# Kernel optimization log

Measured on AMD Instinct MI355X. Metric: run time of the kernel, lower is better.

Reference implementation:

```python
import jax, jax.numpy as jnp
import numpy as np

EPS_CLAMP = 1.0 - 1e-06


def _patch_pool_view(x, H, W, p):
    # x: (n, H*W, s) with spatial flattened row-major over (H, W)
    # -> (n, (H//p)*(W//p), p*p, s), matching einops 'n (h ph w pw) s -> n (h w) (ph pw) s'
    n, q, s = x.shape
    h, w = H // p, W // p
    x = x.reshape(n, h, p, w, p, s)
    x = x.transpose(0, 1, 3, 2, 4, 5)  # n h w ph pw s
    return x.reshape(n, h * w, p * p, s)


def setup_inputs() -> dict:
    key = jax.random.key(0)
    k1, k2 = jax.random.split(key)
    N, C, H, W = 8, 256, 48, 48
    return {
        'mask_feats': jax.random.normal(k1, (N, C, H, W), dtype=jnp.float32),
        'query_feats_all': jax.random.normal(k2, (N, C, H, W), dtype=jnp.float32),
        'path_size': 4,
    }


def reference(mask_feats, query_feats_all, path_size):
    N, c_m, hm, wm = mask_feats.shape
    _, c_q, hq, wq = query_feats_all.shape
    # n c h w -> n (h w) c, scaled by 1/sqrt(c)
    mf = mask_feats.reshape(N, c_m, hm * wm).transpose(0, 2, 1) / (c_m ** 0.5)
    qf = query_feats_all.reshape(N, c_q, hq * wq).transpose(0, 2, 1) / (c_q ** 0.5)
    sim_matrix = jnp.einsum('nqc,nsc->nqs', qf, mf) * 10.0  # (N, Q, S)
    instance_masks = jax.nn.softmax(sim_matrix, axis=1)
    query_masks = jnp.swapaxes(jax.nn.softmax(sim_matrix, axis=2), 1, 2)  # (N, S, Q)
    # patch pooling (computed under torch.no_grad in original)
    tmp_instance_masks_d = jax.lax.stop_gradient(
        _patch_pool_view(instance_masks, hq, wq, path_size))
    instance_masks_d = jnp.minimum(tmp_instance_masks_d.sum(axis=2), EPS_CLAMP)
    tmp_query_masks_d = jax.lax.stop_gradient(
        _patch_pool_view(query_masks, hm, wm, path_size))
    query_masks_d = jnp.minimum(tmp_query_masks_d.sum(axis=2), EPS_CLAMP)
    return (instance_masks, query_masks, instance_masks_d, query_masks_d,
            tmp_instance_masks_d, tmp_query_masks_d)
```

## Files before the change

### kernel.cpp

```cpp
#include <hip/hip_runtime.h>
#include <hip/hip_bf16.h>

#define N_B 8
#define CH 256
#define HW 2304
#define SZ_QS (2304LL*2304LL)
#define SCALE 0.0390625f
#define EPSC 0.999999f
#define QS 512.0f
#define IQS 0.001953125f

typedef __attribute__((ext_vector_type(8))) short bf8_t;
typedef __attribute__((ext_vector_type(8))) unsigned short u16x8;
typedef __attribute__((ext_vector_type(4))) float f32x4;

#define O1 0LL
#define O2 42467328LL
#define O3 84934656LL
#define O4 87588864LL
#define O5 90243072LL
#define O6 132710400LL

__device__ __forceinline__ void gl_lds16(const unsigned short* g, unsigned short* l) {
  __builtin_amdgcn_global_load_lds(
      (const __attribute__((address_space(1))) unsigned int*)g,
      (__attribute__((address_space(3))) unsigned int*)l, 16, 0, 0);
}

__global__ __launch_bounds__(256) void k_tr(const float* __restrict__ q_in,
                                            const float* __restrict__ m_in,
                                            __hip_bfloat16* __restrict__ Abf,
                                            __hip_bfloat16* __restrict__ Bbf,
                                            float* __restrict__ zbuf) {
  __shared__ float lds[64][65];
  const int n = blockIdx.z >> 1, which = blockIdx.z & 1;
  const float* src = which ? m_in : q_in;
  __hip_bfloat16* dst = which ? Bbf : Abf;
  const int q0 = blockIdx.x * 64, c0 = blockIdx.y * 64;
  const int t = threadIdx.x;

  if (zbuf && blockIdx.y == 0 && blockIdx.z == 0) {
    const int i = (blockIdx.x * 256 + t) * 4;
    *(float4*)(zbuf + i) = make_float4(0.f, 0.f, 0.f, 0.f);
  }

  const int cl4 = t >> 4, q4 = (t & 15) * 4;
#pragma unroll
  for (int p = 0; p < 4; ++p) {
    const int cl = p * 16 + cl4;
    const float4 v = *(const float4*)(src + ((size_t)n * CH + c0 + cl) * HW + q0 + q4);
    lds[cl][q4 + 0] = v.x;
    lds[cl][q4 + 1] = v.y;
    lds[cl][q4 + 2] = v.z;
    lds[cl][q4 + 3] = v.w;
  }
  __syncthreads();

  const int c8 = (t & 7) * 8;
#pragma unroll
  for (int p = 0; p < 2; ++p) {
    const int ql = p * 32 + (t >> 3);
    u16x8 o;
#pragma unroll
    for (int k = 0; k < 8; ++k) {
      const __hip_bfloat16 h = __float2bfloat16(lds[c8 + k][ql]);
      o[k] = *(const unsigned short*)&h;
    }
    *(u16x8*)((unsigned short*)dst + ((size_t)n * HW + q0 + ql) * CH + c0 + c8) = o;
  }
}

__global__ __launch_bounds__(256) void k_zero(float* __restrict__ p) {
  const int i = (blockIdx.x * 256 + threadIdx.x) * 4;
  *(float4*)(p + i) = make_float4(0.f, 0.f, 0.f, 0.f);
}

__global__ __launch_bounds__(256) void k_inv(const float* __restrict__ s,
                                             float* __restrict__ inv,
                                             const float scale) {
  const int i = blockIdx.x * 256 + threadIdx.x;
  inv[i] = scale / s[i];
}

__global__ __launch_bounds__(512) void k_p1(
    const unsigned short* __restrict__ Abf, const unsigned short* __restrict__ Bbf,
    float* __restrict__ out1, float* __restrict__ rowsum, float* __restrict__ colsum) {
  __shared__ char smem[49152];
  unsigned short* lA = (unsigned short*)smem;
  unsigned short* lB = (unsigned short*)(smem + 24576);

  const int n = blockIdx.z;
  const int S0 = blockIdx.x * 192, Q0 = blockIdx.y * 192;
  const int t = threadIdx.x, l = t & 63, w = t >> 6;
  const int wm = w >> 2, wn = w & 3;
  const int g = l >> 4, c = l & 15;

  f32x4 acc[6][3];
#pragma unroll
  for (int mi = 0; mi < 6; ++mi)
#pragma unroll
    for (int ni = 0; ni < 3; ++ni) {
      f32x4 z = {0.f, 0.f, 0.f, 0.f};
      acc[mi][ni] = z;
    }

  const int r0w = w * 24;
  const int lrow = l >> 3, lc8 = l & 7;
  const int scol = (lc8 ^ lrow) * 8;
  const unsigned short* gA = Abf + ((size_t)n * HW + Q0 + r0w + lrow) * CH + scol;
  const unsigned short* gB = Bbf + ((size_t)n * HW + S0 + r0w + lrow) * CH + scol;
  unsigned short* dA = lA + r0w * 64;
  unsigned short* dB = lB + r0w * 64;

  for (int kc = 0; kc < 4; ++kc) {
    const int k0 = kc * 64;
    gl_lds16(gA + k0, dA);
    gl_lds16(gA + k0 + 8 * CH, dA + 8 * 64);
    gl_lds16(gA + k0 + 16 * CH, dA + 16 * 64);
    gl_lds16(gB + k0, dB);
    gl_lds16(gB + k0 + 8 * CH, dB + 8 * 64);
    gl_lds16(gB + k0 + 16 * CH, dB + 16 * 64);
    __syncthreads();
#pragma unroll
    for (int ks = 0; ks < 2; ++ks) {
      const int kb = ks * 4 + g;
      bf8_t af[6], bf_[3];
#pragma unroll
      for (int mi = 0; mi < 6; ++mi) {
        const int r = wm * 96 + mi * 16 + c;
        af[mi] = *(const bf8_t*)(lA + r * 64 + ((kb ^ (c & 7)) * 8));
      }
#pragma unroll
      for (int ni = 0; ni < 3; ++ni) {
        const int r = wn * 48 + ni * 16 + c;
        bf_[ni] = *(const bf8_t*)(lB + r * 64 + ((kb ^ (c & 7)) * 8));
      }
#pragma unroll
      for (int mi = 0; mi < 6; ++mi)
#pragma unroll
        for (int ni = 0; ni < 3; ++ni)
          acc[mi][ni] = __builtin_amdgcn_mfma_f32_16x16x32_bf16(af[mi], bf_[ni], acc[mi][ni], 0, 0, 0);
    }
    __syncthreads();
  }

#pragma unroll
  for (int mi = 0; mi < 6; ++mi)
#pragma unroll
    for (int ni = 0; ni < 3; ++ni)
#pragma unroll
      for (int r = 0; r < 4; ++r)
        acc[mi][ni][r] = __expf(acc[mi][ni][r] * SCALE);

  u16x8 ud[9];
#pragma unroll
  for (int mi = 0; mi < 6; ++mi)
#pragma unroll
    for (int ni = 0; ni < 3; ++ni)
#pragma unroll
      for (int r = 0; r < 4; ++r) {
        const int L = mi * 12 + ni * 4 + r;
        ud[L >> 3][L & 7] =
            (unsigned short)fminf(acc[mi][ni][r] * QS + 0.5f, 65535.0f);
      }
  {
    const size_t base = ((size_t)n * HW + Q0) * HW + S0;
#pragma unroll
    for (int j = 0; j < 9; ++j) {
      const int chunk = j * 512 + t;
      const int row = chunk / 48, c16 = chunk % 48;
      *(u16x8*)(out1 + base + (size_t)row * HW + c16 * 4) = ud[j];
    }
  }

#pragma unroll
  for (int mi = 0; mi < 6; ++mi)
#pragma unroll
    for (int r = 0; r < 4; ++r) {
      float v = acc[mi][0][r] + acc[mi][1][r] + acc[mi][2][r];
      v += __shfl_xor(v, 1, 64);
      v += __shfl_xor(v, 2, 64);
      v += __shfl_xor(v, 4, 64);
      v += __shfl_xor(v, 8, 64);
      if (c == 0) atomicAdd(&rowsum[n * HW + Q0 + wm * 96 + mi * 16 + g * 4 + r], v);
    }
#pragma unroll
  for (int ni = 0; ni < 3; ++ni) {
    float v = 0.f;
#pragma unroll
    for (int mi = 0; mi < 6; ++mi)
#pragma unroll
      for (int r = 0; r < 4; ++r) v += acc[mi][ni][r];
    v += __shfl_xor(v, 16, 64);
    v += __shfl_xor(v, 32, 64);
    if (g == 0) atomicAdd(&colsum[n * HW + S0 + wn * 48 + ni * 16 + c], v);
  }
}

__global__ __launch_bounds__(512) void k_p2(
    float* __restrict__ out1, float* __restrict__ out2, float* __restrict__ out3,
    float* __restrict__ out4, float* __restrict__ out5, float* __restrict__ out6,
    const float* __restrict__ rowsum, const float* __restrict__ colsum) {
  __shared__ float fb[48 * 196];
  const int n = blockIdx.z;
  const int bx = blockIdx.x, hq = blockIdx.y;
  const int S0 = bx * 192, Q0 = hq * 192;
  const int t = threadIdx.x, l = t & 63, w = t >> 6;
  const int wm = w >> 2, wn = w & 3;
  const int g = l >> 4, c = l & 15;

  u16x8 ud[9];
  {
    const size_t base = ((size_t)n * HW + Q0) * HW + S0;
#pragma unroll
    for (int j = 0; j < 9; ++j) {
      const int chunk = j * 512 + t;
      const int row = chunk / 48, c16 = chunk % 48;
      ud[j] = *(const u16x8*)(out1 + base + (size_t)row * HW + c16 * 4);
    }
  }
  f32x4 acc[6][3];
#pragma unroll
  for (int mi = 0; mi < 6; ++mi)
#pragma unroll
    for (int ni = 0; ni < 3; ++ni)
#pragma unroll
      for (int r = 0; r < 4; ++r) {
        const int L = mi * 12 + ni * 4 + r;
        acc[mi][ni][r] = (float)ud[L >> 3][L & 7];
      }

  float icv[3];
#pragma unroll
  for (int ni = 0; ni < 3; ++ni)
    icv[ni] = IQS / colsum[n * HW + S0 + wn * 48 + ni * 16 + c];
  f32x4 irv6[6];
#pragma unroll
  for (int mi = 0; mi < 6; ++mi) {
    const int qloc = wm * 96 + mi * 16 + g * 4;
    const f32x4 rs = *(const f32x4*)(rowsum + n * HW + Q0 + qloc);
#pragma unroll
    for (int r = 0; r < 4; ++r) irv6[mi][r] = IQS / rs[r];
  }

#pragma unroll
  for (int ch = 0; ch < 4; ++ch) {
    if (wm == (ch >> 1)) {
#pragma unroll
      for (int m3 = 0; m3 < 3; ++m3) {
        const int mi = (ch & 1) * 3 + m3;
        const int rowb = m3 * 16 + g * 4;
#pragma unroll
        for (int ni = 0; ni < 3; ++ni) {
          const int colb = wn * 48 + ni * 16 + c;
#pragma unroll
          for (int r = 0; r < 4; ++r)
            fb[(rowb + r) * 196 + colb] = acc[mi][ni][r] * icv[ni];
        }
      }
    }
    __syncthreads();
#pragma unroll
    for (int j = 0; j < 5; ++j) {
      const int idx = t + j * 512;
      if (idx < 2304) {
        const int row = idx / 48, col4 = idx % 48;
        const float4 v = *(const float4*)(fb + row * 196 + col4 * 4);
        *(float4*)(out1 + ((size_t)n * HW + Q0 + ch * 48 + row) * HW + S0 + col4 * 4) = v;
        const size_t r5 = ((size_t)n * 144 + hq * 12 + (row >> 2)) * 16 + ch * 4 + (row & 3);
        *(float4*)(out5 + r5 * HW + S0 + col4 * 4) = v;
      }
    }
    __syncthreads();
  }

#pragma unroll
  for (int ch = 0; ch < 4; ++ch) {
    if (wn == ch) {
#pragma unroll
      for (int mi = 0; mi < 6; ++mi) {
        const int colf = wm * 96 + mi * 16 + g * 4;
#pragma unroll
        for (int ni = 0; ni < 3; ++ni) {
          const f32x4 pq = acc[mi][ni] * irv6[mi];
          *(f32x4*)(fb + (ni * 16 + c) * 196 + colf) = pq;
        }
      }
    }
    __syncthreads();
#pragma unroll
    for (int j = 0; j < 5; ++j) {
      const int idx = t + j * 512;
      if (idx < 2304) {
        const int row = idx / 48, col4 = idx % 48;
        const float4 v = *(const float4*)(fb + row * 196 + col4 * 4);
        *(float4*)(out2 + ((size_t)n * HW + S0 + ch * 48 + row) * HW + Q0 + col4 * 4) = v;
        const size_t r6 = ((size_t)n * 144 + bx * 12 + (row >> 2)) * 16 + ch * 4 + (row & 3);
        *(float4*)(out6 + r6 * HW + Q0 + col4 * 4) = v;
      }
    }
    __syncthreads();
  }

#pragma unroll
  for (int m3 = 0; m3 < 3; ++m3) {
    const int b = m3 * 4 + g;
#pragma unroll
    for (int ni = 0; ni < 3; ++ni) {
      const int sl = wn * 48 + ni * 16 + c;
      float p = 0.f;
#pragma unroll
      for (int r = 0; r < 4; ++r) p += acc[m3][ni][r] + acc[m3 + 3][ni][r];
      fb[(wm * 12 + b) * 196 + sl] = p * icv[ni];
    }
  }
  __syncthreads();
#pragma unroll
  for (int j = 0; j < 5; ++j) {
    const int idx = t + j * 512;
    if (idx < 2304) {
      const int b = idx / 192, sl = idx % 192;
      const float v = fb[b * 196 + sl] + fb[(12 + b) * 196 + sl];
      out3[((size_t)n * 144 + hq * 12 + b) * HW + S0 + sl] = fminf(v, EPSC);
    }
  }
  __syncthreads();

#pragma unroll
  for (int mi = 0; mi < 6; ++mi) {
    const int qloc = wm * 96 + mi * 16 + g * 4;
#pragma unroll
    for (int ni = 0; ni < 3; ++ni) {
      f32x4 pq = acc[mi][ni] * irv6[mi];
#pragma unroll
      for (int r = 0; r < 4; ++r) {
        pq[r] += __shfl_xor(pq[r], 1, 64);
        pq[r] += __shfl_xor(pq[r], 2, 64);
      }
      if ((c & 3) == 0) {
        const int pc = ni * 4 + (c >> 2);
        *(f32x4*)(fb + (wn * 12 + pc) * 196 + qloc) = pq;
      }
    }
  }
  __syncthreads();
#pragma unroll
  for (int j = 0; j < 5; ++j) {
    const int idx = t + j * 512;
    if (idx < 2304) {
      const int pc = idx / 192, q = idx % 192;
      const float v = fb[pc * 196 + q] + fb[(12 + pc) * 196 + q] +
                      fb[(24 + pc) * 196 + q] + fb[(36 + pc) * 196 + q];
      out4[((size_t)n * 144 + bx * 12 + pc) * HW + Q0 + q] = fminf(v, EPSC);
    }
  }
}

__global__ __launch_bounds__(256) void k_gemm_old(const unsigned short* __restrict__ Abf,
                                                  const unsigned short* __restrict__ Bbf,
                                                  float* __restrict__ out1,
                                                  float* __restrict__ rowsum,
                                                  float* __restrict__ colsum) {
  __shared__ unsigned short lA[128 * 64];
  __shared__ unsigned short lB[128 * 64];
  const int n = blockIdx.z;
  const int s0 = blockIdx.x * 128, q0 = blockIdx.y * 128;
  const int t = threadIdx.x, l = t & 63, w = t >> 6;
  const int wm = w >> 1, wn = w & 1;
  f32x4 acc[4][4];
#pragma unroll
  for (int mi = 0; mi < 4; ++mi)
#pragma unroll
    for (int ni = 0; ni < 4; ++ni) {
      f32x4 z = {0.f, 0.f, 0.f, 0.f};
      acc[mi][ni] = z;
    }
  const size_t baseA = ((size_t)n * HW + q0) * CH;
  const size_t baseB = ((size_t)n * HW + s0) * CH;
  const int jj = t & 7, rr = t >> 3;
  for (int kc = 0; kc < 4; ++kc) {
    const int k0 = kc * 64;
#pragma unroll
    for (int i = 0; i < 4; ++i) {
      const int r = i * 32 + rr;
      bf8_t va = *(const bf8_t*)(Abf + baseA + (size_t)r * CH + k0 + jj * 8);
      bf8_t vb = *(const bf8_t*)(Bbf + baseB + (size_t)r * CH + k0 + jj * 8);
      *(bf8_t*)(lA + r * 64 + ((jj ^ (r & 7)) * 8)) = va;
      *(bf8_t*)(lB + r * 64 + ((jj ^ (r & 7)) * 8)) = vb;
    }
    __syncthreads();
#pragma unroll
    for (int ks = 0; ks < 2; ++ks) {
      const int kb = ks * 4 + (l >> 4);
      bf8_t af[4], bfr[4];
#pragma unroll
      for (int mi = 0; mi < 4; ++mi) {
        const int r = wm * 64 + mi * 16 + (l & 15);
        af[mi] = *(const bf8_t*)(lA + r * 64 + ((kb ^ (r & 7)) * 8));
      }
#pragma unroll
      for (int ni = 0; ni < 4; ++ni) {
        const int r = wn * 64 + ni * 16 + (l & 15);
        bfr[ni] = *(const bf8_t*)(lB + r * 64 + ((kb ^ (r & 7)) * 8));
      }
#pragma unroll
      for (int mi = 0; mi < 4; ++mi)
#pragma unroll
        for (int ni = 0; ni < 4; ++ni)
          acc[mi][ni] = __builtin_amdgcn_mfma_f32_16x16x32_bf16(af[mi], bfr[ni], acc[mi][ni], 0, 0, 0);
    }
    __syncthreads();
  }
  float rp[4][4], cp[4];
#pragma unroll
  for (int mi = 0; mi < 4; ++mi)
#pragma unroll
    for (int r = 0; r < 4; ++r) rp[mi][r] = 0.f;
#pragma unroll
  for (int ni = 0; ni < 4; ++ni) cp[ni] = 0.f;
#pragma unroll
  for (int mi = 0; mi < 4; ++mi) {
    const int row = q0 + wm * 64 + mi * 16 + (l >> 4) * 4;
#pragma unroll
    for (int ni = 0; ni < 4; ++ni) {
      const int col = s0 + wn * 64 + ni * 16 + (l & 15);
      const size_t ob = ((size_t)n * HW + row) * HW + col;
#pragma unroll
      for (int r = 0; r < 4; ++r) {
        const float e = __expf(acc[mi][ni][r] * SCALE);
        out1[ob + (size_t)r * HW] = e;
        rp[mi][r] += e;
        cp[ni] += e;
      }
    }
  }
#pragma unroll
  for (int mi = 0; mi < 4; ++mi)
#pragma unroll
    for (int r = 0; r < 4; ++r) {
      float v = rp[mi][r];
      v += __shfl_xor(v, 1, 64);
      v += __shfl_xor(v, 2, 64);
      v += __shfl_xor(v, 4, 64);
      v += __shfl_xor(v, 8, 64);
      if ((l & 15) == 0)
        atomicAdd(&rowsum[n * HW + q0 + wm * 64 + mi * 16 + (l >> 4) * 4 + r], v);
    }
#pragma unroll
  for (int ni = 0; ni < 4; ++ni) {
    float v = cp[ni];
    v += __shfl_xor(v, 16, 64);
    v += __shfl_xor(v, 32, 64);
    if (l < 16) atomicAdd(&colsum[n * HW + s0 + wn * 64 + ni * 16 + l], v);
  }
}

__global__ __launch_bounds__(192) void k_main(float* __restrict__ out1,
                                              float* __restrict__ out2,
                                              float* __restrict__ out3,
                                              float* __restrict__ out5,
                                              float* __restrict__ out6,
                                              const float* __restrict__ invr,
                                              const float* __restrict__ invc) {
  __shared__ float ldsT[192 * 49];
  const int n = blockIdx.z, h = blockIdx.y, sb = blockIdx.x;
  const int S0 = sb * 192;
  const int t = threadIdx.x;
  const int sg = S0 + t;
  const float icv = invc[n * HW + sg];
  const float* invr_n = invr + n * HW;
  float* e_base = out1 + (size_t)n * SZ_QS;
  const int Q0 = h * 192;
  float acc[12];
#pragma unroll
  for (int i = 0; i < 12; ++i) acc[i] = 0.f;
  for (int ph = 0; ph < 4; ++ph) {
    const int qf0 = Q0 + ph * 48;
#pragma unroll
    for (int wi = 0; wi < 12; ++wi) {
#pragma unroll
      for (int pw = 0; pw < 4; ++pw) {
        const int col = wi * 4 + pw;
        const int q = qf0 + col;
        const size_t eoff = (size_t)q * HW + sg;
        const float e = e_base[eoff];
        const float pi = e * icv;
        e_base[eoff] = pi;
        out5[((size_t)((n * 144 + h * 12 + wi) * 16 + (ph * 4 + pw))) * HW + sg] = pi;
        acc[wi] += pi;
        ldsT[t * 49 + col] = e * invr_n[q];
      }
    }
    __syncthreads();
    const int u = t & 3, sB = t >> 2;
#pragma unroll
    for (int pass = 0; pass < 4; ++pass) {
      const int sl = pass * 48 + sB;
      const int sgl = S0 + sl;
      const int rs_ = sgl / 48, cs = sgl % 48;
      const int sp = (rs_ >> 2) * 12 + (cs >> 2);
      const int spp = (rs_ & 3) * 4 + (cs & 3);
      const size_t o2row = ((size_t)n * HW + sgl) * HW + qf0;
      const size_t o6row = (((size_t)n * 144 + sp) * 16 + spp) * HW + qf0;
#pragma unroll
      for (int k = 0; k < 3; ++k) {
        const int slot = u + k * 4;
        float4 v;
        v.x = ldsT[sl * 49 + slot * 4 + 0];
        v.y = ldsT[sl * 49 + slot * 4 + 1];
        v.z = ldsT[sl * 49 + slot * 4 + 2];
        v.w = ldsT[sl * 49 + slot * 4 + 3];
        *(float4*)(out2 + o2row + slot * 4) = v;
        *(float4*)(out6 + o6row + slot * 4) = v;
      }
    }
    __syncthreads();
  }
#pragma unroll
  for (int wi = 0; wi < 12; ++wi)
    out3[((size_t)(n * 144 + h * 12 + wi)) * HW + sg] = fminf(acc[wi], EPSC);
}

__global__ __launch_bounds__(256) void k_qd(const float* __restrict__ out6,
                                            float* __restrict__ out4) {
  const int n = blockIdx.y, sp = blockIdx.x;
  const float* b6 = out6 + (((size_t)n * 144 + sp) * 16) * HW;
  float* b4 = out4 + ((size_t)n * 144 + sp) * HW;
  for (int i = 0; i < 9; ++i) {
    const int qq = i * 256 + threadIdx.x;
    float s = 0.f;
#pragma unroll
    for (int spp = 0; spp < 16; ++spp) s += b6[(size_t)spp * HW + qq];
    b4[qq] = fminf(s, EPSC);
  }
}

extern "C" void kernel_launch(void* const* d_in, const int* in_sizes, int n_in,
                              void* d_out, int out_size, void* d_ws, size_t ws_size,
                              hipStream_t stream) {
  const float* mask_f = (const float*)d_in[0];
  const float* query_f = (const float*)d_in[1];
  float* out = (float*)d_out;
  float* out1 = out + O1;
  float* out2 = out + O2;
  float* out3 = out + O3;
  float* out4 = out + O4;
  float* out5 = out + O5;
  float* out6 = out + O6;

  const size_t abytes = (size_t)N_B * HW * CH * 2;
  const size_t sbytes = (size_t)N_B * HW * 4;
  const size_t need = 2 * abytes + 4 * sbytes;

  if (ws_size >= need) {
    char* base = (char*)d_ws;
    __hip_bfloat16* Abf = (__hip_bfloat16*)base;
    __hip_bfloat16* Bbf = (__hip_bfloat16*)(base + abytes);
    float* sums = (float*)(base + 2 * abytes);
    float* rowsum = sums;
    float* colsum = sums + N_B * HW;

    k_tr<<<dim3(36, 4, 16), 256, 0, stream>>>(query_f, mask_f, Abf, Bbf, sums);
    k_p1<<<dim3(12, 12, 8), 512, 0, stream>>>(
        (const unsigned short*)Abf, (const unsigned short*)Bbf, out1, rowsum, colsum);
    k_p2<<<dim3(12, 12, 8), 512, 0, stream>>>(out1, out2, out3, out4, out5, out6,
                                              rowsum, colsum);
  } else {
    __hip_bfloat16* Abf = (__hip_bfloat16*)out4;
    __hip_bfloat16* Bbf = (__hip_bfloat16*)out3;
    float* sums = (float*)((char*)out4 + abytes);
    float* invs = sums + 2 * (N_B * HW);
    float* rowsum = sums;
    float* colsum = sums + N_B * HW;
    float* invr = invs;
    float* invc = invs + N_B * HW;

    k_tr<<<dim3(36, 4, 16), 256, 0, stream>>>(query_f, mask_f, Abf, Bbf, nullptr);
    k_zero<<<dim3(36), 256, 0, stream>>>(sums);
    k_gemm_old<<<dim3(18, 18, 8), 256, 0, stream>>>(
        (const unsigned short*)Abf, (const unsigned short*)Bbf, out1, rowsum, colsum);
    k_inv<<<dim3(144), 256, 0, stream>>>(sums, invs, 1.0f);
    k_main<<<dim3(12, 12, 8), 192, 0, stream>>>(out1, out2, out3, out5, out6, invr, invc);
    k_qd<<<dim3(144, 8), 256, 0, stream>>>(out6, out4);
  }
}
```

Measured before the change: 243.2 us.

## Double-buffer LDS staging in the similarity GEMM with K-step prefetch

Replaces the single-buffered 64-wide K chunk loop in k_p1 with a double-buffered 32-wide K pipeline. The next step's global-to-LDS loads are issued before the current step's MFMAs, and the LDS swizzle is reworked for the narrower rows. The goal is to overlap global load latency with matrix compute and cut from two barriers per chunk to one. In exchange there are twice as many, smaller steps, and correctness now depends on async LDS loads into the other buffer not racing with reads.

```diff
diff --git a/kernel.cpp b/kernel.cpp
--- a/kernel.cpp
+++ b/kernel.cpp
@@ -85,9 +85,7 @@
 __global__ __launch_bounds__(512) void k_p1(
     const unsigned short* __restrict__ Abf, const unsigned short* __restrict__ Bbf,
     float* __restrict__ out1, float* __restrict__ rowsum, float* __restrict__ colsum) {
-  __shared__ char smem[49152];
-  unsigned short* lA = (unsigned short*)smem;
-  unsigned short* lB = (unsigned short*)(smem + 24576);
+  __shared__ unsigned short smem[4 * 192 * 32];
 
   const int n = blockIdx.z;
   const int S0 = blockIdx.x * 192, Q0 = blockIdx.y * 192;
@@ -104,45 +102,62 @@
       acc[mi][ni] = z;
     }
 
-  const int r0w = w * 24;
-  const int lrow = l >> 3, lc8 = l & 7;
-  const int scol = (lc8 ^ lrow) * 8;
-  const unsigned short* gA = Abf + ((size_t)n * HW + Q0 + r0w + lrow) * CH + scol;
-  const unsigned short* gB = Bbf + ((size_t)n * HW + S0 + r0w + lrow) * CH + scol;
-  unsigned short* dA = lA + r0w * 64;
-  unsigned short* dB = lB + r0w * 64;
-
-  for (int kc = 0; kc < 4; ++kc) {
-    const int k0 = kc * 64;
-    gl_lds16(gA + k0, dA);
-    gl_lds16(gA + k0 + 8 * CH, dA + 8 * 64);
-    gl_lds16(gA + k0 + 16 * CH, dA + 16 * 64);
-    gl_lds16(gB + k0, dB);
-    gl_lds16(gB + k0 + 8 * CH, dB + 8 * 64);
-    gl_lds16(gB + k0 + 16 * CH, dB + 16 * 64);
-    __syncthreads();
-#pragma unroll
-    for (int ks = 0; ks < 2; ++ks) {
-      const int kb = ks * 4 + g;
-      bf8_t af[6], bf_[3];
-#pragma unroll
-      for (int mi = 0; mi < 6; ++mi) {
-        const int r = wm * 96 + mi * 16 + c;
-        af[mi] = *(const bf8_t*)(lA + r * 64 + ((kb ^ (c & 7)) * 8));
-      }
-#pragma unroll
-      for (int ni = 0; ni < 3; ++ni) {
-        const int r = wn * 48 + ni * 16 + c;
-        bf_[ni] = *(const bf8_t*)(lB + r * 64 + ((kb ^ (c & 7)) * 8));
-      }
-#pragma unroll
-      for (int mi = 0; mi < 6; ++mi)
-#pragma unroll
-        for (int ni = 0; ni < 3; ++ni)
-          acc[mi][ni] = __builtin_amdgcn_mfma_f32_16x16x32_bf16(af[mi], bf_[ni], acc[mi][ni], 0, 0, 0);
-    }
-    __syncthreads();
-  }
+  const int rrel = l >> 2;
+  const int sseg = (l & 3) ^ ((l >> 3) & 3);
+  const unsigned short* gAb = Abf + ((size_t)n * HW + Q0) * CH;
+  const unsigned short* gBb = Bbf + ((size_t)n * HW + S0) * CH;
+  const int ch0 = w * 3, ch1 = w * 3 + 1, ch2 = w * 3 + 2;
+
+#define STAGE_CHUNK(chv, buf, k0)                                              \
+  {                                                                            \
+    const int isA = (chv) < 12;                                                \
+    const int crel = isA ? (chv) : (chv)-12;                                   \
+    const unsigned short* sp_ =                                                \
+        (isA ? gAb : gBb) + (size_t)(crel * 16 + rrel) * CH + (k0) + sseg * 8; \
+    unsigned short* dp_ = smem + (buf)*12288 + (isA ? 0 : 6144) + crel * 512;  \
+    gl_lds16(sp_, dp_);                                                        \
+  }
+
+#define STAGE_STEP(buf, step)                  \
+  {                                            \
+    const int k0_ = (step)*32;                 \
+    STAGE_CHUNK(ch0, buf, k0_);                \
+    STAGE_CHUNK(ch1, buf, k0_);                \
+    STAGE_CHUNK(ch2, buf, k0_);                \
+  }
+
+  STAGE_STEP(0, 0);
+  __syncthreads();
+
+  int cur = 0;
+#pragma unroll 2
+  for (int step = 0; step < 8; ++step) {
+    if (step < 7) STAGE_STEP(cur ^ 1, step + 1);
+    const unsigned short* lA = smem + cur * 12288;
+    const unsigned short* lB = lA + 6144;
+    bf8_t af[6], bf_[3];
+#pragma unroll
+    for (int mi = 0; mi < 6; ++mi) {
+      const int r = wm * 96 + mi * 16 + c;
+      const int sg_ = g ^ ((c >> 1) & 3);
+      af[mi] = *(const bf8_t*)(lA + r * 32 + sg_ * 8);
+    }
+#pragma unroll
+    for (int ni = 0; ni < 3; ++ni) {
+      const int r = wn * 48 + ni * 16 + c;
+      const int sg_ = g ^ ((c >> 1) & 3);
+      bf_[ni] = *(const bf8_t*)(lB + r * 32 + sg_ * 8);
+    }
+#pragma unroll
+    for (int mi = 0; mi < 6; ++mi)
+#pragma unroll
+      for (int ni = 0; ni < 3; ++ni)
+        acc[mi][ni] = __builtin_amdgcn_mfma_f32_16x16x32_bf16(af[mi], bf_[ni], acc[mi][ni], 0, 0, 0);
+    __syncthreads();
+    cur ^= 1;
+  }
+#undef STAGE_CHUNK
+#undef STAGE_STEP
 
 #pragma unroll
   for (int mi = 0; mi < 6; ++mi)
```

Result: faster. 224.1 us (-7.8%).
